# Performance work log

Hardware: AMD Instinct MI355X
Metric: run time of the kernel (lower is better)

Reference implementation:

```python
import jax, jax.numpy as jnp
import numpy as np

H_BANDWIDTH = 0.5
EPS = 1e-5


def setup_inputs() -> dict:
    key = jax.random.key(0)
    k1, k2 = jax.random.split(key)
    x = jax.random.normal(k1, (4, 256, 64, 64), dtype=jnp.float32)
    y = jax.random.normal(k2, (4, 256, 64, 64), dtype=jnp.float32)
    return {"x": x, "y": y}


def reference(x, y):
    # x, y: (N, C, H, W), H=W=64 so no pooling branch is taken
    N, C, H, W = x.shape
    # mean over batch and spatial dims of y -> per-channel mu, shape (1, C, 1, 1)
    y_mu = jnp.mean(y, axis=(0, 2, 3)).reshape(1, C, 1, 1)
    x_c = x - y_mu
    y_c = y - y_mu
    # L2-normalize over channel dim
    x_n = x_c / jnp.linalg.norm(x_c, axis=1, keepdims=True)
    y_n = y_c / jnp.linalg.norm(y_c, axis=1, keepdims=True)
    x_n = x_n.reshape(N, C, H * W)
    y_n = y_n.reshape(N, C, H * W)
    # cosine similarity: (N, HW, HW)
    cos = jnp.einsum("ncp,ncq->npq", x_n, y_n)
    d = 1.0 - cos
    d_min = jnp.min(d, axis=2, keepdims=True)
    d_tilde = d / (d_min + EPS)
    w = jnp.exp((1.0 - d_tilde) / H_BANDWIDTH)
    cx_ij = w / jnp.sum(w, axis=2, keepdims=True)
    cx = jnp.mean(jnp.max(cx_ij, axis=1), axis=1)  # (N,)
    cx_loss = jnp.mean(-jnp.log(cx + EPS))
    return cx_loss
```

## Files before the change

kernel.cpp:

```cpp
#include <hip/hip_runtime.h>
#include <hip/hip_bf16.h>

typedef short bf16x8 __attribute__((ext_vector_type(8)));
typedef float f32x4 __attribute__((ext_vector_type(4)));

#define NB 4
#define C 256
#define HW 4096
#define NROWS (NB * HW)
#define EPSF 1e-5f

__device__ __forceinline__ unsigned short f2bf(float f) {
    unsigned int u = __float_as_uint(f);
    unsigned int r = u + 0x7fffu + ((u >> 16) & 1u);
    return (unsigned short)(r >> 16);
}
__device__ __forceinline__ float bf2f(unsigned int h) {
    return __uint_as_float(h << 16);
}
__device__ __forceinline__ void unpack8(uint4 u, float* v) {
    unsigned int w0 = u.x, w1 = u.y, w2 = u.z, w3 = u.w;
    v[0] = bf2f(w0 & 0xffffu); v[1] = bf2f(w0 >> 16);
    v[2] = bf2f(w1 & 0xffffu); v[3] = bf2f(w1 >> 16);
    v[4] = bf2f(w2 & 0xffffu); v[5] = bf2f(w2 >> 16);
    v[6] = bf2f(w3 & 0xffffu); v[7] = bf2f(w3 >> 16);
}
__device__ __forceinline__ float waveReduceSum(float v) {
    for (int off = 32; off > 0; off >>= 1) v += __shfl_xor(v, off);
    return v;
}
typedef __attribute__((address_space(1))) const unsigned int glb_cu;
typedef __attribute__((address_space(3))) unsigned int lds_u;
__device__ __forceinline__ void async_copy16(const unsigned short* g, unsigned short* l) {
    __builtin_amdgcn_global_load_lds((glb_cu*)g, (lds_u*)l, 16, 0, 0);
}

__global__ __launch_bounds__(256) void mu_kernel(const float* __restrict__ y,
                                                 float* __restrict__ mu) {
    int c = blockIdx.x;
    int tid = threadIdx.x;
    float s = 0.f;
    const float* base = y + (size_t)c * HW;
    for (int n = 0; n < NB; n++) {
        const float* bn = base + (size_t)n * C * HW;
        for (int i = tid; i < HW; i += 256) s += bn[i];
    }
    s = waveReduceSum(s);
    __shared__ float red[4];
    int lane = tid & 63, wave = tid >> 6;
    if (lane == 0) red[wave] = s;
    __syncthreads();
    if (tid == 0) mu[c] = (red[0] + red[1] + red[2] + red[3]) * (1.0f / 16384.0f);
}

#define TP 32
#define TSTRIDE 257
__global__ __launch_bounds__(256) void prep_kernel(const float* __restrict__ x,
                                                   const float* __restrict__ y,
                                                   const float* __restrict__ mu,
                                                   unsigned short* __restrict__ Xn,
                                                   unsigned short* __restrict__ Yn) {
    __shared__ float smu[C];
    __shared__ float tile[TP * TSTRIDE];
    __shared__ float red[8 * 32];
    __shared__ float invn[TP];
    int tid = threadIdx.x;
    smu[tid] = mu[tid];
    int blk = blockIdx.x;
    int n = blk >> 7;
    int p0 = (blk & 127) * TP;
    int tp = tid & 31, cc = tid >> 5;
    __syncthreads();
    for (int pass = 0; pass < 2; pass++) {
        const float* in = pass ? y : x;
        unsigned short* out = pass ? Yn : Xn;
        const float* base = in + (size_t)n * C * HW + p0 + tp;
        float ssq = 0.f;
        for (int c = cc; c < C; c += 8) {
            float v = base[(size_t)c * HW] - smu[c];
            tile[tp * TSTRIDE + c] = v;
            ssq += v * v;
        }
        red[cc * 32 + tp] = ssq;
        __syncthreads();
        if (tid < 32) {
            float s = 0.f;
            for (int k = 0; k < 8; k++) s += red[k * 32 + tid];
            invn[tid] = rsqrtf(s);
        }
        __syncthreads();
        int c2 = (tid & 127) * 2;
        int pp = tid >> 7;
        for (int p = pp; p < TP; p += 2) {
            float inv = invn[p];
            unsigned short b0 = f2bf(tile[p * TSTRIDE + c2] * inv);
            unsigned short b1 = f2bf(tile[p * TSTRIDE + c2 + 1] * inv);
            unsigned int pack = (unsigned int)b0 | ((unsigned int)b1 << 16);
            ((unsigned int*)out)[(size_t)(n * HW + p0 + p) * (C / 2) + (c2 >> 1)] = pack;
        }
        __syncthreads();
    }
}

#define EPSTRIDE 136
__global__ __launch_bounds__(256, 2) void gemm_cos(const unsigned short* __restrict__ Xn,
                                                   const unsigned short* __restrict__ Yn,
                                                   unsigned short* __restrict__ Cos) {
    __shared__ unsigned short lds_us[32768];
    int n = blockIdx.z;
    int pBase = blockIdx.y * 128, qBase = blockIdx.x * 128;
    const unsigned short* Ab = Xn + ((size_t)n * HW + pBase) * C;
    const unsigned short* Bb = Yn + ((size_t)n * HW + qBase) * C;
    int tid = threadIdx.x, lane = tid & 63, wave = tid >> 6;
    int wm = (wave >> 1) * 64, wn = (wave & 1) * 64;
    int mrow = lane & 15, quad = lane >> 4;

    f32x4 acc[4][4];
#pragma unroll
    for (int i = 0; i < 4; i++)
#pragma unroll
        for (int j = 0; j < 4; j++) acc[i][j] = (f32x4){0.f, 0.f, 0.f, 0.f};

#pragma unroll
    for (int h = 0; h < 2; h++) {
#pragma unroll
        for (int mat = 0; mat < 2; mat++) {
            const unsigned short* g = mat ? Bb : Ab;
            unsigned short* lbase = lds_us + mat * 16384;
#pragma unroll
            for (int t = 0; t < 8; t++) {
                int slot = t * 256 + tid;
                int r = slot >> 4, cl = slot & 15;
                int c = h * 16 + (cl ^ (r & 15));
                async_copy16(g + (size_t)r * C + c * 8, lbase + slot * 8);
            }
        }
        __syncthreads();
#pragma unroll
        for (int kkl = 0; kkl < 4; kkl++) {
            int cl4 = kkl * 4 + quad;
            int clp = cl4 ^ mrow;
            bf16x8 af[4], bfr[4];
#pragma unroll
            for (int i = 0; i < 4; i++) {
                af[i]  = *(const bf16x8*)(lds_us + (wm + i * 16 + mrow) * 128 + clp * 8);
                bfr[i] = *(const bf16x8*)(lds_us + 16384 + (wn + i * 16 + mrow) * 128 + clp * 8);
            }
#pragma unroll
            for (int i = 0; i < 4; i++)
#pragma unroll
                for (int j = 0; j < 4; j++)
                    acc[i][j] = __builtin_amdgcn_mfma_f32_16x16x32_bf16(af[i], bfr[j], acc[i][j], 0, 0, 0);
        }
        __syncthreads();
    }

    unsigned short* epb = lds_us;
    int col = lane & 15, quad4 = quad * 4;
#pragma unroll
    for (int i = 0; i < 4; i++)
#pragma unroll
        for (int j = 0; j < 4; j++)
#pragma unroll
            for (int r = 0; r < 4; r++)
                epb[(wm + i * 16 + quad4 + r) * EPSTRIDE + wn + j * 16 + col] = f2bf(acc[i][j][r]);
    __syncthreads();
    unsigned short* Crow = Cos + (size_t)n * HW * HW;
#pragma unroll
    for (int it = 0; it < 8; it++) {
        int e = it * 2048 + tid * 8;
        int r = e >> 7, cg = e & 127;
        uint4 o = *(const uint4*)(epb + r * EPSTRIDE + cg);
        *(uint4*)(Crow + (size_t)(pBase + r) * HW + qBase + cg) = o;
    }
}

__global__ __launch_bounds__(256, 3) void rowcol(const unsigned short* __restrict__ Cos,
                                                 unsigned short* __restrict__ partial) {
    int n = blockIdx.y, chunk = blockIdx.x;
    int tid = threadIdx.x, lane = tid & 63, wave = tid >> 6;
    const unsigned short* rowbase = Cos + ((size_t)n * HW + chunk * 8) * HW;
    __shared__ float redm[8][4];
    __shared__ float sval[8][4];

    uint4 d[8][2];
#pragma unroll
    for (int r = 0; r < 8; r++) {
        const unsigned short* rp = rowbase + (size_t)r * HW;
        d[r][0] = *(const uint4*)(rp + tid * 8);
        d[r][1] = *(const uint4*)(rp + 2048 + tid * 8);
    }

    float m8[8];
#pragma unroll
    for (int r = 0; r < 8; r++) {
        float v[16];
        unpack8(d[r][0], v); unpack8(d[r][1], v + 8);
        float m = v[0];
#pragma unroll
        for (int k = 1; k < 16; k++) m = fmaxf(m, v[k]);
        m8[r] = m;
    }
#pragma unroll
    for (int off = 32; off > 0; off >>= 1)
#pragma unroll
        for (int r = 0; r < 8; r++) m8[r] = fmaxf(m8[r], __shfl_xor(m8[r], off));
    if (lane == 0)
#pragma unroll
        for (int r = 0; r < 8; r++) redm[r][wave] = m8[r];
    __syncthreads();

    float alpha[8], basec[8];
#pragma unroll
    for (int r = 0; r < 8; r++) {
        float M = fmaxf(fmaxf(redm[r][0], redm[r][1]), fmaxf(redm[r][2], redm[r][3]));
        alpha[r] = 2.0f / ((1.0f - M) + EPSF);
        basec[r] = 2.0f - alpha[r];
    }

    float s8[8];
#pragma unroll
    for (int r = 0; r < 8; r++) {
        float v[16];
        unpack8(d[r][0], v); unpack8(d[r][1], v + 8);
        float s = 0.f;
#pragma unroll
        for (int k = 0; k < 16; k++) s += __expf(fmaf(alpha[r], v[k], basec[r]));
        s8[r] = s;
    }
#pragma unroll
    for (int off = 32; off > 0; off >>= 1)
#pragma unroll
        for (int r = 0; r < 8; r++) s8[r] += __shfl_xor(s8[r], off);
    if (lane == 0)
#pragma unroll
        for (int r = 0; r < 8; r++) sval[r][wave] = s8[r];
    __syncthreads();

    float cmax[16];
#pragma unroll
    for (int k = 0; k < 16; k++) cmax[k] = -1e30f;
#pragma unroll
    for (int r = 0; r < 8; r++) {
        float S = sval[r][0] + sval[r][1] + sval[r][2] + sval[r][3];
        float beta = basec[r] - __logf(S);
        float v[16];
        unpack8(d[r][0], v); unpack8(d[r][1], v + 8);
#pragma unroll
        for (int k = 0; k < 16; k++) cmax[k] = fmaxf(cmax[k], fmaf(alpha[r], v[k], beta));
    }

    unsigned short* outp = partial + ((size_t)(n * 512 + chunk)) * HW;
    uint4 o0, o1;
    o0.x = (unsigned int)f2bf(cmax[0]) | ((unsigned int)f2bf(cmax[1]) << 16);
    o0.y = (unsigned int)f2bf(cmax[2]) | ((unsigned int)f2bf(cmax[3]) << 16);
    o0.z = (unsigned int)f2bf(cmax[4]) | ((unsigned int)f2bf(cmax[5]) << 16);
    o0.w = (unsigned int)f2bf(cmax[6]) | ((unsigned int)f2bf(cmax[7]) << 16);
    o1.x = (unsigned int)f2bf(cmax[8]) | ((unsigned int)f2bf(cmax[9]) << 16);
    o1.y = (unsigned int)f2bf(cmax[10]) | ((unsigned int)f2bf(cmax[11]) << 16);
    o1.z = (unsigned int)f2bf(cmax[12]) | ((unsigned int)f2bf(cmax[13]) << 16);
    o1.w = (unsigned int)f2bf(cmax[14]) | ((unsigned int)f2bf(cmax[15]) << 16);
    *(uint4*)(outp + tid * 8) = o0;
    *(uint4*)(outp + 2048 + tid * 8) = o1;
}

__global__ __launch_bounds__(256) void colmax1(const unsigned short* __restrict__ partial,
                                               float* __restrict__ partial2) {
    int n = blockIdx.z, cg = blockIdx.y;
    int q0 = blockIdx.x * 2048 + threadIdx.x * 8;
    const unsigned short* p = partial + ((size_t)(n * 512 + cg * 32)) * HW + q0;
    float mx[8];
#pragma unroll
    for (int k = 0; k < 8; k++) mx[k] = -1e30f;
    for (int c = 0; c < 32; c++) {
        uint4 u = *(const uint4*)(p + (size_t)c * HW);
        float v[8];
        unpack8(u, v);
#pragma unroll
        for (int k = 0; k < 8; k++) mx[k] = fmaxf(mx[k], v[k]);
    }
    float* o = partial2 + ((size_t)(n * 16 + cg)) * HW + q0;
#pragma unroll
    for (int k = 0; k < 8; k += 4) {
        float4 ov = {mx[k], mx[k + 1], mx[k + 2], mx[k + 3]};
        *(float4*)(o + k) = ov;
    }
}

__global__ __launch_bounds__(1024) void colfinal2(const float* __restrict__ partial2,
                                                  float* __restrict__ cxsum) {
    int n = blockIdx.x;
    int tid = threadIdx.x;
    const float* p = partial2 + (size_t)n * 16 * HW + tid * 4;
    float4 m = {-1e30f, -1e30f, -1e30f, -1e30f};
#pragma unroll
    for (int g = 0; g < 16; g++) {
        float4 v = *(const float4*)(p + (size_t)g * HW);
        m.x = fmaxf(m.x, v.x); m.y = fmaxf(m.y, v.y);
        m.z = fmaxf(m.z, v.z); m.w = fmaxf(m.w, v.w);
    }
    float s = __expf(m.x) + __expf(m.y) + __expf(m.z) + __expf(m.w);
    s = waveReduceSum(s);
    __shared__ float red[16];
    int lane = tid & 63, wave = tid >> 6;
    if (lane == 0) red[wave] = s;
    __syncthreads();
    if (tid == 0) {
        float S = 0.f;
        for (int w = 0; w < 16; w++) S += red[w];
        cxsum[n] = S;
    }
}

__global__ void finalize(const float* __restrict__ cxsum, float* __restrict__ out) {
    if (threadIdx.x == 0 && blockIdx.x == 0) {
        float loss = 0.f;
        for (int n = 0; n < NB; n++) {
            float cx = cxsum[n] * (1.0f / 4096.0f);
            loss += -logf(cx + EPSF);
        }
        out[0] = loss * 0.25f;
    }
}

extern "C" void kernel_launch(void* const* d_in, const int* in_sizes, int n_in,
                              void* d_out, int out_size, void* d_ws, size_t ws_size,
                              hipStream_t stream) {
    const float* x = (const float*)d_in[0];
    const float* y = (const float*)d_in[1];
    float* out = (float*)d_out;
    char* ws = (char*)d_ws;

    float* mu               = (float*)(ws + 0);
    float* cxsum            = (float*)(ws + 1024);
    float* partial2         = (float*)(ws + 65536);
    unsigned short* Xn      = (unsigned short*)(ws + 2097152);
    unsigned short* Yn      = (unsigned short*)(ws + 10485760);
    unsigned short* partial = (unsigned short*)(ws + 2097152);
    unsigned short* Cos     = (unsigned short*)(ws + 18874368);

    mu_kernel<<<C, 256, 0, stream>>>(y, mu);
    prep_kernel<<<NROWS / TP, 256, 0, stream>>>(x, y, mu, Xn, Yn);
    gemm_cos<<<dim3(HW / 128, HW / 128, NB), 256, 0, stream>>>(Xn, Yn, Cos);
    rowcol<<<dim3(512, NB), 256, 0, stream>>>(Cos, partial);
    colmax1<<<dim3(2, 16, NB), 256, 0, stream>>>(partial, partial2);
    colfinal2<<<NB, 1024, 0, stream>>>(partial2, cxsum);
    finalize<<<1, 64, 0, stream>>>(cxsum, out);
}
```

Before: 201.4 us.

## Double-buffer GEMM K-loop with 64-wide stages to overlap loads and MFMA

Replaces the two-step K loop, which loaded 128 columns per step and then synchronized, with four 64-column stages in two LDS buffers. The load for the next stage is issued before the MFMA work on the current buffer, so global-to-LDS copies overlap with compute. The XOR swizzle is reduced to an 8-chunk pattern to match the narrower rows. This adds more barriers and smaller copy batches per stage, and the pipeline depth is limited to four stages because K is only 256.

```diff
diff --git a/kernel.cpp b/kernel.cpp
--- a/kernel.cpp
+++ b/kernel.cpp
@@ -103,6 +103,48 @@
 }
 
 #define EPSTRIDE 136
+#define STAGE(s, b)                                                            \
+    do {                                                                       \
+        unsigned short* lA = lds_us + (b) * 16384;                             \
+        unsigned short* lB = lds_us + (b) * 16384 + 8192;                      \
+        _Pragma("unroll")                                                      \
+        for (int t = 0; t < 4; t++) {                                          \
+            int slot = t * 256 + tid;                                          \
+            int r = slot >> 3, cl = slot & 7;                                  \
+            int c = (s) * 8 + (cl ^ (r & 7));                                  \
+            async_copy16(Ab + (size_t)r * C + c * 8, lA + slot * 8);           \
+        }                                                                      \
+        _Pragma("unroll")                                                      \
+        for (int t = 0; t < 4; t++) {                                          \
+            int slot = t * 256 + tid;                                          \
+            int r = slot >> 3, cl = slot & 7;                                  \
+            int c = (s) * 8 + (cl ^ (r & 7));                                  \
+            async_copy16(Bb + (size_t)r * C + c * 8, lB + slot * 8);           \
+        }                                                                      \
+    } while (0)
+
+#define COMPUTE(b)                                                             \
+    do {                                                                       \
+        const unsigned short* lA = lds_us + (b) * 16384;                       \
+        const unsigned short* lB = lds_us + (b) * 16384 + 8192;                \
+        _Pragma("unroll")                                                      \
+        for (int kkl = 0; kkl < 2; kkl++) {                                    \
+            int cl4 = kkl * 4 + quad;                                          \
+            int clp = cl4 ^ (mrow & 7);                                        \
+            bf16x8 af[4], bfr[4];                                              \
+            _Pragma("unroll")                                                  \
+            for (int i = 0; i < 4; i++) {                                      \
+                af[i]  = *(const bf16x8*)(lA + (wm + i * 16 + mrow) * 64 + clp * 8); \
+                bfr[i] = *(const bf16x8*)(lB + (wn + i * 16 + mrow) * 64 + clp * 8); \
+            }                                                                  \
+            _Pragma("unroll")                                                  \
+            for (int i = 0; i < 4; i++)                                        \
+                _Pragma("unroll")                                              \
+                for (int j = 0; j < 4; j++)                                    \
+                    acc[i][j] = __builtin_amdgcn_mfma_f32_16x16x32_bf16(af[i], bfr[j], acc[i][j], 0, 0, 0); \
+        }                                                                      \
+    } while (0)
+
 __global__ __launch_bounds__(256, 2) void gemm_cos(const unsigned short* __restrict__ Xn,
                                                    const unsigned short* __restrict__ Yn,
                                                    unsigned short* __restrict__ Cos) {
@@ -121,39 +163,19 @@
 #pragma unroll
         for (int j = 0; j < 4; j++) acc[i][j] = (f32x4){0.f, 0.f, 0.f, 0.f};
 
-#pragma unroll
-    for (int h = 0; h < 2; h++) {
-#pragma unroll
-        for (int mat = 0; mat < 2; mat++) {
-            const unsigned short* g = mat ? Bb : Ab;
-            unsigned short* lbase = lds_us + mat * 16384;
-#pragma unroll
-            for (int t = 0; t < 8; t++) {
-                int slot = t * 256 + tid;
-                int r = slot >> 4, cl = slot & 15;
-                int c = h * 16 + (cl ^ (r & 15));
-                async_copy16(g + (size_t)r * C + c * 8, lbase + slot * 8);
-            }
-        }
+    STAGE(0, 0);
+    __syncthreads();
+
+#pragma unroll
+    for (int s = 0; s < 3; s++) {
+        STAGE(s + 1, (s + 1) & 1);
+        __builtin_amdgcn_sched_barrier(0);
+        COMPUTE(s & 1);
         __syncthreads();
-#pragma unroll
-        for (int kkl = 0; kkl < 4; kkl++) {
-            int cl4 = kkl * 4 + quad;
-            int clp = cl4 ^ mrow;
-            bf16x8 af[4], bfr[4];
-#pragma unroll
-            for (int i = 0; i < 4; i++) {
-                af[i]  = *(const bf16x8*)(lds_us + (wm + i * 16 + mrow) * 128 + clp * 8);
-                bfr[i] = *(const bf16x8*)(lds_us + 16384 + (wn + i * 16 + mrow) * 128 + clp * 8);
-            }
-#pragma unroll
-            for (int i = 0; i < 4; i++)
-#pragma unroll
-                for (int j = 0; j < 4; j++)
-                    acc[i][j] = __builtin_amdgcn_mfma_f32_16x16x32_bf16(af[i], bfr[j], acc[i][j], 0, 0, 0);
-        }
-        __syncthreads();
-    }
+    }
+
+    COMPUTE(1);
+    __syncthreads();
 
     unsigned short* epb = lds_us;
     int col = lane & 15, quad4 = quad * 4;
```

Result: no change. 200.9 us (-0.2%).
